# Optimization experiments

Measured on AMD Instinct MI355X. Metric: run time of the kernel, lower is better.

The kernel has to match this reference:

```python
import jax, jax.numpy as jnp
import numpy as np
from jax import lax

B, UD, YD, ZD, H, L, T = 256, 16, 16, 32, 128, 2, 2048


def _lin_params(key, out_dim, in_dim):
    k1, k2 = jax.random.split(key)
    s = 1.0 / np.sqrt(in_dim)
    w = jax.random.uniform(k1, (out_dim, in_dim), minval=-s, maxval=s, dtype=jnp.float32)
    b = jax.random.uniform(k2, (out_dim,), minval=-s, maxval=s, dtype=jnp.float32)
    return w, b


def setup_inputs() -> dict:
    key = jax.random.key(0)
    ks = iter(jax.random.split(key, 24))
    d = {}
    d["u"] = jax.random.normal(next(ks), (B, UD, T), dtype=jnp.float32)
    d["y"] = jax.random.normal(next(ks), (B, YD, T), dtype=jnp.float32)
    d["h0"] = jax.random.uniform(next(ks), (L, B, H), dtype=jnp.float32)  # torch.rand init
    d["phi_u_w1"], d["phi_u_b1"] = _lin_params(next(ks), H, UD)
    d["phi_u_w2"], d["phi_u_b2"] = _lin_params(next(ks), H, H)
    d["dynn_w1"], d["dynn_b1"] = _lin_params(next(ks), H, 2 * H)
    d["dynn_w2"], d["dynn_b2"] = _lin_params(next(ks), H, H)
    d["x_mean_w"], d["x_mean_b"] = _lin_params(next(ks), ZD, H)
    d["phi_x_w1"], d["phi_x_b1"] = _lin_params(next(ks), H, ZD)
    d["phi_x_w2"], d["phi_x_b2"] = _lin_params(next(ks), H, H)
    d["menn_w1"], d["menn_b1"] = _lin_params(next(ks), H, H)
    d["menn_w2"], d["menn_b2"] = _lin_params(next(ks), YD, H)
    s = 1.0 / np.sqrt(H)
    d["gru_wih"] = jax.random.uniform(next(ks), (L, 3 * H, H), minval=-s, maxval=s, dtype=jnp.float32)
    d["gru_whh"] = jax.random.uniform(next(ks), (L, 3 * H, H), minval=-s, maxval=s, dtype=jnp.float32)
    return d


def _mlp(x, w1, b1, w2, b2):
    # Linear -> ReLU -> Linear (torch Linear convention: x @ W.T + b)
    return jax.nn.relu(x @ w1.T + b1) @ w2.T + b2


def _gru_step(h, x_in, wih, whh):
    # h: (L, B, H); x_in: (B, H); nn.GRU with bias=False
    new_h = []
    inp = x_in
    for l in range(L):
        gi = inp @ wih[l].T           # (B, 3H)
        gh = h[l] @ whh[l].T          # (B, 3H)
        i_r, i_z, i_n = jnp.split(gi, 3, axis=-1)
        h_r, h_z, h_n = jnp.split(gh, 3, axis=-1)
        r = jax.nn.sigmoid(i_r + h_r)
        z = jax.nn.sigmoid(i_z + h_z)
        n = jnp.tanh(i_n + r * h_n)
        hl = (1.0 - z) * n + z * h[l]
        new_h.append(hl)
        inp = hl
    return jnp.stack(new_h)


def reference(u, y, h0, phi_u_w1, phi_u_b1, phi_u_w2, phi_u_b2,
              dynn_w1, dynn_b1, dynn_w2, dynn_b2, x_mean_w, x_mean_b,
              phi_x_w1, phi_x_b1, phi_x_w2, phi_x_b2,
              menn_w1, menn_b1, menn_w2, menn_b2, gru_wih, gru_whh):
    # mpnt_wt = -1 branch (0 >= mpnt_wt > -10): pure NN dynamics + measurement
    u_t = jnp.transpose(u, (2, 0, 1))  # (T, B, UD)
    y_t = jnp.transpose(y, (2, 0, 1))  # (T, B, YD)
    # phi_u has no recurrent dependency -> precompute over all timesteps
    pu = _mlp(u_t, phi_u_w1, phi_u_b1, phi_u_w2, phi_u_b2)  # (T, B, H)

    def step(h, inputs):
        pu_t, yt = inputs
        d = _mlp(jnp.concatenate([pu_t, h[-1]], axis=1), dynn_w1, dynn_b1, dynn_w2, dynn_b2)
        x_t = d @ x_mean_w.T + x_mean_b                 # (B, ZD)
        h_new = _gru_step(h, pu_t, gru_wih, gru_whh)
        px = _mlp(x_t, phi_x_w1, phi_x_b1, phi_x_w2, phi_x_b2)
        y_hat = _mlp(px, menn_w1, menn_b1, menn_w2, menn_b2)
        loss_t = jnp.sum((y_hat - yt) ** 2)
        return h_new, loss_t

    _, losses = lax.scan(step, h0, (pu, y_t))
    return jnp.sum(losses)
```

## Files before the change

kernel.cpp:

```cpp
#include <hip/hip_runtime.h>
#include <hip/hip_bf16.h>

#define TT 2048
#define BB 256
#define HH 128
#define UDIM 16
#define YDIM 16
#define ZDIM 32
#define H3 384

typedef __hip_bfloat16 bf16;
typedef _Float16 half2v __attribute__((ext_vector_type(2)));

constexpr int clog2(int x) { return x <= 1 ? 0 : 1 + clog2(x >> 1); }

template <int M_, int K_, int O_, bool RELU_>
__device__ __forceinline__ void rstage(const float* __restrict__ wfrag,
                                       const float* __restrict__ xin, int XS,
                                       float* __restrict__ ps,
                                       const float* __restrict__ bias,
                                       float* __restrict__ outb)
{
    constexpr int F = K_ / O_;
    const int T = threadIdx.x;
    const int jb = T & (M_ / 2 - 1);
    const int o  = T >> clog2(M_ / 2);
#pragma unroll
    for (int r = 0; r < 8; ++r) {
        float a0 = 0.f, a1 = 0.f;
#pragma unroll
        for (int g = 0; g < F; g += 4) {
            const float4 xv = *reinterpret_cast<const float4*>(&xin[r * XS + o * F + g]);
            a0 += xv.x * wfrag[g]     + xv.y * wfrag[g + 1]
                + xv.z * wfrag[g + 2] + xv.w * wfrag[g + 3];
            a1 += xv.x * wfrag[F + g]     + xv.y * wfrag[F + g + 1]
                + xv.z * wfrag[F + g + 2] + xv.w * wfrag[F + g + 3];
        }
        ps[r * 1024 + o * M_ + jb]           = a0;
        ps[r * 1024 + o * M_ + jb + M_ / 2]  = a1;
    }
    __syncthreads();
    for (int oi = T; oi < 8 * M_; oi += 512) {
        const int r = oi >> clog2(M_);
        const int j = oi & (M_ - 1);
        float s = bias[j];
#pragma unroll
        for (int o2 = 0; o2 < O_; ++o2) s += ps[r * 1024 + o2 * M_ + j];
        if (RELU_) s = fmaxf(s, 0.f);
        outb[r * M_ + j] = s;
    }
    __syncthreads();
}

template <int M_, int K_, int O_>
__device__ __forceinline__ void loadw(float* __restrict__ wfrag, const float* __restrict__ Wg)
{
    constexpr int F = K_ / O_;
    const int T = threadIdx.x;
    const int jb = T & (M_ / 2 - 1);
    const int o  = T >> clog2(M_ / 2);
#pragma unroll
    for (int h = 0; h < 2; ++h)
#pragma unroll
        for (int g = 0; g < F; g += 4)
            *reinterpret_cast<float4*>(&wfrag[h * F + g]) =
                *reinterpret_cast<const float4*>(&Wg[(jb + h * (M_ / 2)) * K_ + o * F + g]);
}

template <int M_, int K_, int O_>
__device__ __forceinline__ void loadw_h(half2v* __restrict__ wfrag, const float* __restrict__ Wg)
{
    constexpr int F = K_ / O_;
    const int T = threadIdx.x;
    const int jb = T & (M_ / 2 - 1);
    const int o  = T >> clog2(M_ / 2);
#pragma unroll
    for (int h = 0; h < 2; ++h)
#pragma unroll
        for (int g = 0; g < F / 2; ++g) {
            const float* s = &Wg[(jb + h * (M_ / 2)) * K_ + o * F + 2 * g];
            half2v v; v.x = (_Float16)s[0]; v.y = (_Float16)s[1];
            wfrag[h * (F / 2) + g] = v;
        }
}

template <int M_, int K_, int O_, bool RELU_>
__device__ __forceinline__ void rstage_h(const half2v* __restrict__ wfrag,
                                         const _Float16* __restrict__ xin, int XS,
                                         float* __restrict__ ps,
                                         const float* __restrict__ bias,
                                         _Float16* __restrict__ outb)
{
    constexpr int F = K_ / O_;
    constexpr int FH = F / 2;
    const int T = threadIdx.x;
    const int jb = T & (M_ / 2 - 1);
    const int o  = T >> clog2(M_ / 2);
#pragma unroll
    for (int r = 0; r < 8; ++r) {
        float a0 = 0.f, a1 = 0.f;
        const half2v* xv = reinterpret_cast<const half2v*>(xin + r * XS + o * F);
        if constexpr (FH >= 4) {
#pragma unroll
            for (int g4 = 0; g4 < FH / 4; ++g4) {
                half2v xt[4];
                *reinterpret_cast<float4*>(xt) = reinterpret_cast<const float4*>(xv)[g4];
#pragma unroll
                for (int e = 0; e < 4; ++e) {
                    a0 = __builtin_amdgcn_fdot2(xt[e], wfrag[g4 * 4 + e], a0, false);
                    a1 = __builtin_amdgcn_fdot2(xt[e], wfrag[FH + g4 * 4 + e], a1, false);
                }
            }
        } else {
            half2v xt[2];
            *reinterpret_cast<float2*>(xt) = *reinterpret_cast<const float2*>(xv);
            a0 = __builtin_amdgcn_fdot2(xt[0], wfrag[0], a0, false);
            a0 = __builtin_amdgcn_fdot2(xt[1], wfrag[1], a0, false);
            a1 = __builtin_amdgcn_fdot2(xt[0], wfrag[FH], a1, false);
            a1 = __builtin_amdgcn_fdot2(xt[1], wfrag[FH + 1], a1, false);
        }
        ps[r * 1024 + o * M_ + jb]           = a0;
        ps[r * 1024 + o * M_ + jb + M_ / 2]  = a1;
    }
    __syncthreads();
    for (int oi = T; oi < 8 * M_; oi += 512) {
        const int r = oi >> clog2(M_);
        const int j = oi & (M_ - 1);
        float s = bias[j];
#pragma unroll
        for (int o2 = 0; o2 < O_; ++o2) s += ps[r * 1024 + o2 * M_ + j];
        if (RELU_) s = fmaxf(s, 0.f);
        outb[r * M_ + j] = (_Float16)s;
    }
    __syncthreads();
}

__global__ __launch_bounds__(512, 2) void phi_u_kernel(
    const float* __restrict__ u, const float* __restrict__ w1, const float* __restrict__ b1,
    const float* __restrict__ w2, const float* __restrict__ b2,
    bf16* __restrict__ pu, int s0, int nrows)
{
    __shared__ __align__(16) float ps[8192];
    __shared__ __align__(16) float xc[8 * 16];
    __shared__ __align__(16) float bP[8 * 128];
    __shared__ __align__(16) float bias_l[256];
    const int T = threadIdx.x;
    if (T < 128) { bias_l[T] = b1[T]; bias_l[128 + T] = b2[T]; }
    const int jb = T & 63, o = T >> 6;
    float wa[4];
    wa[0] = w1[jb * 16 + o * 2];        wa[1] = w1[jb * 16 + o * 2 + 1];
    wa[2] = w1[(jb + 64) * 16 + o * 2]; wa[3] = w1[(jb + 64) * 16 + o * 2 + 1];
    float wb[32]; loadw<128, 128, 8>(wb, w2);
    __syncthreads();

    for (int tile = blockIdx.x; tile < nrows / 32; tile += gridDim.x) {
        const int n0 = tile * 32;
        const int b  = s0 + (n0 >> 11);
        const int t0 = n0 & (TT - 1);
#pragma unroll 1
        for (int rb = 0; rb < 4; ++rb) {
            if (T < 128) {
                const int r = T & 7, c = T >> 3;
                xc[r * 16 + c] = u[((size_t)b * UDIM + c) * TT + t0 + rb * 8 + r];
            }
            __syncthreads();
#pragma unroll
            for (int r = 0; r < 8; ++r) {
                const float x0 = xc[r * 16 + o * 2], x1 = xc[r * 16 + o * 2 + 1];
                ps[r * 1024 + o * 128 + jb]      = x0 * wa[0] + x1 * wa[1];
                ps[r * 1024 + o * 128 + jb + 64] = x0 * wa[2] + x1 * wa[3];
            }
            __syncthreads();
            for (int oi = T; oi < 8 * 128; oi += 512) {
                const int r = oi >> 7, j = oi & 127;
                float s = bias_l[j];
#pragma unroll
                for (int o2 = 0; o2 < 8; ++o2) s += ps[r * 1024 + o2 * 128 + j];
                bP[r * 128 + j] = fmaxf(s, 0.f);
            }
            __syncthreads();
            rstage<128, 128, 8, false>(wb, bP, 128, ps, bias_l + 128, bP);
            const int row0 = n0 + rb * 8;
            for (int oi = T; oi < 8 * 128; oi += 512) {
                const int r = oi >> 7, j = oi & 127;
                pu[(size_t)(row0 + r) * HH + j] = __float2bfloat16(bP[r * 128 + j]);
            }
            __syncthreads();
        }
    }
}

__device__ __forceinline__ void gmv(const half2v w[6][16], const _Float16* __restrict__ vb,
                                    int o, float* __restrict__ psL, int psb)
{
    const half2v* vec2 = reinterpret_cast<const half2v*>(vb) + o * 16;
    float a0 = 0.f, a1 = 0.f, a2 = 0.f, a3 = 0.f, a4 = 0.f, a5 = 0.f;
#pragma unroll
    for (int k4 = 0; k4 < 4; ++k4) {
        half2v xt[4];
        *reinterpret_cast<float4*>(xt) = reinterpret_cast<const float4*>(vec2)[k4];
#pragma unroll
        for (int e = 0; e < 4; ++e) {
            const int k = k4 * 4 + e;
            a0 = __builtin_amdgcn_fdot2(xt[e], w[0][k], a0, false);
            a1 = __builtin_amdgcn_fdot2(xt[e], w[1][k], a1, false);
            a2 = __builtin_amdgcn_fdot2(xt[e], w[2][k], a2, false);
            a3 = __builtin_amdgcn_fdot2(xt[e], w[3][k], a3, false);
            a4 = __builtin_amdgcn_fdot2(xt[e], w[4][k], a4, false);
            a5 = __builtin_amdgcn_fdot2(xt[e], w[5][k], a5, false);
        }
    }
    psL[psb]       = a0; psL[psb + 64]  = a1; psL[psb + 128] = a2;
    psL[psb + 192] = a3; psL[psb + 256] = a4; psL[psb + 320] = a5;
}

__global__ __launch_bounds__(512, 2) void gru_fused_kernel(
    const bf16* __restrict__ pu_in,
    const float* __restrict__ wih,
    const float* __restrict__ whh,
    const float* __restrict__ h0_g,
    bf16* __restrict__ hlast,
    int s0)
{
    const int t = threadIdx.x;
    __shared__ __align__(16) _Float16 x0h[HH];
    __shared__ __align__(16) _Float16 x1h[2][HH];
    __shared__ __align__(16) _Float16 h0h[HH];
    __shared__ __align__(16) _Float16 h1h[HH];
    __shared__ __align__(16) float ps[2 * 3072];

    const int g = t >> 6;
    const int m = g >> 2, o = g & 3;
    const int u = t & 63;
    const float* WbaseA = ((m == 0) ? wih : whh);
    const float* WbaseB = WbaseA + (size_t)H3 * HH;
    half2v wA[6][16], wB[6][16];
#pragma unroll
    for (int i = 0; i < 6; ++i) {
        const float* sA = &WbaseA[(u + 64 * i) * HH + o * 32];
        const float* sB = &WbaseB[(u + 64 * i) * HH + o * 32];
#pragma unroll
        for (int k = 0; k < 16; ++k) {
            half2v v; v.x = (_Float16)sA[2 * k]; v.y = (_Float16)sA[2 * k + 1];
            wA[i][k] = v;
            half2v w2; w2.x = (_Float16)sB[2 * k]; w2.y = (_Float16)sB[2 * k + 1];
            wB[i][k] = w2;
        }
    }
    float* psA = ps;
    float* psB = ps + 3072;
    const int psb = o * 768 + m * 384 + u;

    const bf16* xb = pu_in + (size_t)blockIdx.x * TT * HH;
    bf16* ob = hlast + (size_t)blockIdx.x * TT * HH;

    float hreg = 0.f;
    if (t < HH) {
        hreg = h0_g[(size_t)(s0 + blockIdx.x) * HH + t];
        h0h[t] = (_Float16)hreg;
        x0h[t] = (_Float16)__bfloat162float(xb[t]);
    } else if (t < 2 * HH) {
        const int j = t - HH;
        hreg = h0_g[((size_t)BB + s0 + blockIdx.x) * HH + j];
        h1h[j] = (_Float16)hreg;
    }
    __syncthreads();

#pragma unroll 1
    for (int i = 0; i <= TT; ++i) {
        float xnext = 0.f;
        if (t < HH && i + 1 < TT)
            xnext = __bfloat162float(xb[(size_t)(i + 1) * HH + t]);
        if (i < TT)  gmv(wA, (m == 0) ? x0h : h0h, o, psA, psb);
        if (i >= 1)  gmv(wB, (m == 0) ? x1h[(i + 1) & 1] : h1h, o, psB, psb);
        __syncthreads();
        if (t < HH) {
            if (i < TT) {
                const int j = t;
                float gir = 0.f, giz = 0.f, gin = 0.f, ghr = 0.f, ghz = 0.f, ghn = 0.f;
#pragma unroll
                for (int o2 = 0; o2 < 4; ++o2) {
                    const float* pp = psA + o2 * 768;
                    gir += pp[j];        giz += pp[128 + j]; gin += pp[256 + j];
                    ghr += pp[384 + j];  ghz += pp[512 + j]; ghn += pp[640 + j];
                }
                const float rg = 1.f / (1.f + __expf(-(gir + ghr)));
                const float zg = 1.f / (1.f + __expf(-(giz + ghz)));
                const float narg = gin + rg * ghn;
                const float e2 = __expf(2.f * fabsf(narg));
                float ng = 1.f - 2.f / (e2 + 1.f);
                ng = (narg < 0.f) ? -ng : ng;
                const float hn = (1.f - zg) * ng + zg * hreg;
                h0h[j] = (_Float16)hn;
                x1h[i & 1][j] = (_Float16)hn;
                x0h[j] = (_Float16)xnext;
                hreg = hn;
            }
        } else if (t < 2 * HH) {
            if (i >= 1) {
                const int j = t - HH;
                float gir = 0.f, giz = 0.f, gin = 0.f, ghr = 0.f, ghz = 0.f, ghn = 0.f;
#pragma unroll
                for (int o2 = 0; o2 < 4; ++o2) {
                    const float* pp = psB + o2 * 768;
                    gir += pp[j];        giz += pp[128 + j]; gin += pp[256 + j];
                    ghr += pp[384 + j];  ghz += pp[512 + j]; ghn += pp[640 + j];
                }
                const float rg = 1.f / (1.f + __expf(-(gir + ghr)));
                const float zg = 1.f / (1.f + __expf(-(giz + ghz)));
                const float narg = gin + rg * ghn;
                const float e2 = __expf(2.f * fabsf(narg));
                float ng = 1.f - 2.f / (e2 + 1.f);
                ng = (narg < 0.f) ? -ng : ng;
                ob[(size_t)(i - 1) * HH + j] = __float2bfloat16(hreg);
                const float hn = (1.f - zg) * ng + zg * hreg;
                h1h[j] = (_Float16)hn;
                hreg = hn;
            }
        }
        __syncthreads();
    }
}

__device__ __forceinline__ void stage_xc_h(_Float16* __restrict__ xc,
                                           const bf16* __restrict__ pu,
                                           const bf16* __restrict__ hl,
                                           int n0, int rb)
{
    const int T = threadIdx.x;
    const int base = n0 + rb * 8;
#pragma unroll
    for (int i = 0; i < 4; ++i) {
        const int idx = T + i * 512;
        const int r = idx >> 8, k = idx & 255;
        const size_t row = (size_t)(base + r);
        xc[r * 256 + k] = (_Float16)((k < 128) ? __bfloat162float(pu[row * HH + k])
                                               : __bfloat162float(hl[row * HH + (k - 128)]));
    }
}

__global__ __launch_bounds__(512, 2) void head_kernel(
    const bf16* __restrict__ pu, const bf16* __restrict__ hlast, const float* __restrict__ y_g,
    const float* __restrict__ dw1, const float* __restrict__ db1,
    const float* __restrict__ dw2, const float* __restrict__ db2,
    const float* __restrict__ xw, const float* __restrict__ xb,
    const float* __restrict__ pxw1, const float* __restrict__ pxb1,
    const float* __restrict__ pxw2, const float* __restrict__ pxb2,
    const float* __restrict__ mw1, const float* __restrict__ mb1,
    const float* __restrict__ mw2, const float* __restrict__ mb2,
    float* __restrict__ out, int s0, int nrows)
{
    __shared__ __align__(16) float ps[8192];
    __shared__ __align__(16) _Float16 xc[8 * 256];
    __shared__ __align__(16) _Float16 bP[8 * 128];
    __shared__ __align__(16) _Float16 bQ[8 * 128];
    __shared__ __align__(16) _Float16 bX[8 * 32];
    __shared__ __align__(16) float bias_l[688];
    __shared__ float red[8];
    const int T = threadIdx.x;

    if (T < 128) bias_l[T]       = db1[T];
    if (T < 128) bias_l[128 + T] = db2[T];
    if (T < 32)  bias_l[256 + T] = xb[T];
    if (T < 128) bias_l[288 + T] = pxb1[T];
    if (T < 128) bias_l[416 + T] = pxb2[T];
    if (T < 128) bias_l[544 + T] = mb1[T];
    if (T < 16)  bias_l[672 + T] = mb2[T];

    half2v w1[32]; loadw_h<128, 256, 8 >(w1, dw1);
    half2v w2[16]; loadw_h<128, 128, 8 >(w2, dw2);
    half2v w3[4];  loadw_h<32,  128, 32>(w3, xw);
    half2v w4[4];  loadw_h<128, 32,  8 >(w4, pxw1);
    half2v w5[16]; loadw_h<128, 128, 8 >(w5, pxw2);
    half2v w6[16]; loadw_h<128, 128, 8 >(w6, mw1);
    const int jb7 = T & 7, o7 = T >> 3;
    half2v w7a, w7b;
    w7a.x = (_Float16)mw2[jb7 * 128 + 2 * o7];
    w7a.y = (_Float16)mw2[jb7 * 128 + 2 * o7 + 1];
    w7b.x = (_Float16)mw2[(jb7 + 8) * 128 + 2 * o7];
    w7b.y = (_Float16)mw2[(jb7 + 8) * 128 + 2 * o7 + 1];

    float lossreg = 0.f;

    for (int tile = blockIdx.x; tile < nrows / 32; tile += gridDim.x) {
        const int n0 = tile * 32;
        const int b  = s0 + (n0 >> 11);
        const int t0 = n0 & (TT - 1);
        stage_xc_h(xc, pu, hlast, n0, 0);
#pragma unroll 1
        for (int rb = 0; rb < 4; ++rb) {
            __syncthreads();
            rstage_h<128, 256, 8,  true >(w1, xc, 256, ps, bias_l + 0,   bP);
            rstage_h<128, 128, 8,  false>(w2, bP, 128, ps, bias_l + 128, bQ);
            rstage_h<32,  128, 32, false>(w3, bQ, 128, ps, bias_l + 256, bX);
            rstage_h<128, 32,  8,  true >(w4, bX, 32,  ps, bias_l + 288, bP);
            rstage_h<128, 128, 8,  false>(w5, bP, 128, ps, bias_l + 416, bQ);
            rstage_h<128, 128, 8,  true >(w6, bQ, 128, ps, bias_l + 544, bP);
#pragma unroll
            for (int r = 0; r < 8; ++r) {
                const half2v xv = *reinterpret_cast<const half2v*>(&bP[r * 128 + 2 * o7]);
                ps[r * 1024 + o7 * 16 + jb7]     = __builtin_amdgcn_fdot2(xv, w7a, 0.f, false);
                ps[r * 1024 + o7 * 16 + jb7 + 8] = __builtin_amdgcn_fdot2(xv, w7b, 0.f, false);
            }
            if (rb < 3) stage_xc_h(xc, pu, hlast, n0, rb + 1);
            __syncthreads();
            if (T < 128) {
                const int r = T >> 4, j = T & 15;
                float s = bias_l[672 + j];
#pragma unroll
                for (int o2 = 0; o2 < 64; ++o2) s += ps[r * 1024 + o2 * 16 + j];
                const int trow = t0 + rb * 8 + r;
                const float yv = y_g[((size_t)b * YDIM + j) * TT + trow];
                const float d = s - yv;
                lossreg += d * d;
            }
        }
    }
    __syncthreads();
#pragma unroll
    for (int off = 32; off > 0; off >>= 1) lossreg += __shfl_down(lossreg, off, 64);
    if ((T & 63) == 0) red[T >> 6] = lossreg;
    __syncthreads();
    if (T == 0) {
        float s = 0.f;
#pragma unroll
        for (int i = 0; i < 8; ++i) s += red[i];
        atomicAdd(out, s);
    }
}

__global__ void zero_out_kernel(float* o) { o[0] = 0.f; }

extern "C" void kernel_launch(void* const* d_in, const int* in_sizes, int n_in,
                              void* d_out, int out_size, void* d_ws, size_t ws_size,
                              hipStream_t stream)
{
    (void)in_sizes; (void)n_in; (void)out_size;
    const float* u    = (const float*)d_in[0];
    const float* y    = (const float*)d_in[1];
    const float* h0   = (const float*)d_in[2];
    const float* puw1 = (const float*)d_in[3];
    const float* pub1 = (const float*)d_in[4];
    const float* puw2 = (const float*)d_in[5];
    const float* pub2 = (const float*)d_in[6];
    const float* dw1  = (const float*)d_in[7];
    const float* db1  = (const float*)d_in[8];
    const float* dw2  = (const float*)d_in[9];
    const float* db2  = (const float*)d_in[10];
    const float* xw   = (const float*)d_in[11];
    const float* xbi  = (const float*)d_in[12];
    const float* pxw1 = (const float*)d_in[13];
    const float* pxb1 = (const float*)d_in[14];
    const float* pxw2 = (const float*)d_in[15];
    const float* pxb2 = (const float*)d_in[16];
    const float* mw1  = (const float*)d_in[17];
    const float* mb1  = (const float*)d_in[18];
    const float* mw2  = (const float*)d_in[19];
    const float* mb2  = (const float*)d_in[20];
    const float* gwih = (const float*)d_in[21];
    const float* gwhh = (const float*)d_in[22];

    const size_t per_sample = (size_t)TT * HH * 2 * 2;
    int C = BB;
    while (C > 1 && (size_t)C * per_sample > ws_size) C >>= 1;
    bf16* puB = (bf16*)d_ws;
    bf16* hlB = puB + (size_t)C * TT * HH;

    zero_out_kernel<<<1, 1, 0, stream>>>((float*)d_out);
    for (int s0 = 0; s0 < BB; s0 += C) {
        phi_u_kernel<<<512, 512, 0, stream>>>(u, puw1, pub1, puw2, pub2, puB, s0, C * TT);
        gru_fused_kernel<<<C, 512, 0, stream>>>(puB, gwih, gwhh, h0, hlB, s0);
        head_kernel<<<512, 512, 0, stream>>>(puB, hlB, y,
                                             dw1, db1, dw2, db2, xw, xbi,
                                             pxw1, pxb1, pxw2, pxb2,
                                             mw1, mb1, mw2, mb2,
                                             (float*)d_out, s0, C * TT);
    }
}
```

Before: 4.888 ms.

## Replace shared-memory partial-sum reductions with wavefront shuffle reductions

```diff
diff --git a/kernel.cpp b/kernel.cpp
--- a/kernel.cpp
+++ b/kernel.cpp
@@ -68,69 +68,87 @@
 }
 
 template <int M_, int K_, int O_>
-__device__ __forceinline__ void loadw_h(half2v* __restrict__ wfrag, const float* __restrict__ Wg)
+__device__ __forceinline__ void loadw_s(half2v* __restrict__ wfrag, const float* __restrict__ Wg)
 {
     constexpr int F = K_ / O_;
-    const int T = threadIdx.x;
-    const int jb = T & (M_ / 2 - 1);
-    const int o  = T >> clog2(M_ / 2);
-#pragma unroll
-    for (int h = 0; h < 2; ++h)
-#pragma unroll
-        for (int g = 0; g < F / 2; ++g) {
-            const float* s = &Wg[(jb + h * (M_ / 2)) * K_ + o * F + 2 * g];
-            half2v v; v.x = (_Float16)s[0]; v.y = (_Float16)s[1];
-            wfrag[h * (F / 2) + g] = v;
-        }
+    constexpr int FH = F / 2;
+    constexpr int LO = clog2(O_);
+    const int T = threadIdx.x;
+    const int o  = T & (O_ - 1);
+    const int jb = T >> LO;
+#pragma unroll
+    for (int h = 0; h < 2; ++h) {
+        const float* src = Wg + (size_t)(jb + h * (M_ / 2)) * K_;
+        if constexpr (F >= 8) {
+            constexpr int NS = F / 8;
+#pragma unroll
+            for (int s = 0; s < NS; ++s)
+#pragma unroll
+                for (int e = 0; e < 4; ++e) {
+                    const float* p = src + o * 8 + s * (8 * O_) + 2 * e;
+                    half2v v; v.x = (_Float16)p[0]; v.y = (_Float16)p[1];
+                    wfrag[h * FH + s * 4 + e] = v;
+                }
+        } else {
+#pragma unroll
+            for (int e = 0; e < 2; ++e) {
+                const float* p = src + o * 4 + 2 * e;
+                half2v v; v.x = (_Float16)p[0]; v.y = (_Float16)p[1];
+                wfrag[h * FH + e] = v;
+            }
+        }
+    }
 }
 
 template <int M_, int K_, int O_, bool RELU_>
-__device__ __forceinline__ void rstage_h(const half2v* __restrict__ wfrag,
+__device__ __forceinline__ void rstage_s(const half2v* __restrict__ wfrag,
                                          const _Float16* __restrict__ xin, int XS,
-                                         float* __restrict__ ps,
                                          const float* __restrict__ bias,
                                          _Float16* __restrict__ outb)
 {
     constexpr int F = K_ / O_;
     constexpr int FH = F / 2;
-    const int T = threadIdx.x;
-    const int jb = T & (M_ / 2 - 1);
-    const int o  = T >> clog2(M_ / 2);
+    constexpr int LO = clog2(O_);
+    const int T = threadIdx.x;
+    const int o  = T & (O_ - 1);
+    const int jb = T >> LO;
 #pragma unroll
     for (int r = 0; r < 8; ++r) {
         float a0 = 0.f, a1 = 0.f;
-        const half2v* xv = reinterpret_cast<const half2v*>(xin + r * XS + o * F);
-        if constexpr (FH >= 4) {
-#pragma unroll
-            for (int g4 = 0; g4 < FH / 4; ++g4) {
+        if constexpr (F >= 8) {
+            constexpr int NS = F / 8;
+#pragma unroll
+            for (int s = 0; s < NS; ++s) {
                 half2v xt[4];
-                *reinterpret_cast<float4*>(xt) = reinterpret_cast<const float4*>(xv)[g4];
+                *reinterpret_cast<float4*>(xt) =
+                    *reinterpret_cast<const float4*>(xin + r * XS + o * 8 + s * (8 * O_));
 #pragma unroll
                 for (int e = 0; e < 4; ++e) {
-                    a0 = __builtin_amdgcn_fdot2(xt[e], wfrag[g4 * 4 + e], a0, false);
-                    a1 = __builtin_amdgcn_fdot2(xt[e], wfrag[FH + g4 * 4 + e], a1, false);
+                    a0 = __builtin_amdgcn_fdot2(xt[e], wfrag[s * 4 + e], a0, false);
+                    a1 = __builtin_amdgcn_fdot2(xt[e], wfrag[FH + s * 4 + e], a1, false);
                 }
             }
         } else {
             half2v xt[2];
-            *reinterpret_cast<float2*>(xt) = *reinterpret_cast<const float2*>(xv);
+            *reinterpret_cast<float2*>(xt) =
+                *reinterpret_cast<const float2*>(xin + r * XS + o * 4);
             a0 = __builtin_amdgcn_fdot2(xt[0], wfrag[0], a0, false);
             a0 = __builtin_amdgcn_fdot2(xt[1], wfrag[1], a0, false);
             a1 = __builtin_amdgcn_fdot2(xt[0], wfrag[FH], a1, false);
             a1 = __builtin_amdgcn_fdot2(xt[1], wfrag[FH + 1], a1, false);
         }
-        ps[r * 1024 + o * M_ + jb]           = a0;
-        ps[r * 1024 + o * M_ + jb + M_ / 2]  = a1;
-    }
-    __syncthreads();
-    for (int oi = T; oi < 8 * M_; oi += 512) {
-        const int r = oi >> clog2(M_);
-        const int j = oi & (M_ - 1);
-        float s = bias[j];
-#pragma unroll
-        for (int o2 = 0; o2 < O_; ++o2) s += ps[r * 1024 + o2 * M_ + j];
-        if (RELU_) s = fmaxf(s, 0.f);
-        outb[r * M_ + j] = (_Float16)s;
+#pragma unroll
+        for (int s = 1; s < O_; s <<= 1) {
+            a0 += __shfl_xor(a0, s, 64);
+            a1 += __shfl_xor(a1, s, 64);
+        }
+        if (o == 0) {
+            float s0 = a0 + bias[jb];
+            float s1 = a1 + bias[jb + M_ / 2];
+            if (RELU_) { s0 = fmaxf(s0, 0.f); s1 = fmaxf(s1, 0.f); }
+            outb[r * M_ + jb]          = (_Float16)s0;
+            outb[r * M_ + jb + M_ / 2] = (_Float16)s1;
+        }
     }
     __syncthreads();
 }
@@ -190,11 +208,11 @@
     }
 }
 
-__device__ __forceinline__ void gmv(const half2v w[6][16], const _Float16* __restrict__ vb,
-                                    int o, float* __restrict__ psL, int psb)
+__device__ __forceinline__ void gmv_s(const half2v w[6][16], const _Float16* __restrict__ vb,
+                                      int o, float* __restrict__ a)
 {
     const half2v* vec2 = reinterpret_cast<const half2v*>(vb) + o * 16;
-    float a0 = 0.f, a1 = 0.f, a2 = 0.f, a3 = 0.f, a4 = 0.f, a5 = 0.f;
+    a[0] = 0.f; a[1] = 0.f; a[2] = 0.f; a[3] = 0.f; a[4] = 0.f; a[5] = 0.f;
 #pragma unroll
     for (int k4 = 0; k4 < 4; ++k4) {
         half2v xt[4];
@@ -202,16 +220,19 @@
 #pragma unroll
         for (int e = 0; e < 4; ++e) {
             const int k = k4 * 4 + e;
-            a0 = __builtin_amdgcn_fdot2(xt[e], w[0][k], a0, false);
-            a1 = __builtin_amdgcn_fdot2(xt[e], w[1][k], a1, false);
-            a2 = __builtin_amdgcn_fdot2(xt[e], w[2][k], a2, false);
-            a3 = __builtin_amdgcn_fdot2(xt[e], w[3][k], a3, false);
-            a4 = __builtin_amdgcn_fdot2(xt[e], w[4][k], a4, false);
-            a5 = __builtin_amdgcn_fdot2(xt[e], w[5][k], a5, false);
-        }
-    }
-    psL[psb]       = a0; psL[psb + 64]  = a1; psL[psb + 128] = a2;
-    psL[psb + 192] = a3; psL[psb + 256] = a4; psL[psb + 320] = a5;
+            a[0] = __builtin_amdgcn_fdot2(xt[e], w[0][k], a[0], false);
+            a[1] = __builtin_amdgcn_fdot2(xt[e], w[1][k], a[1], false);
+            a[2] = __builtin_amdgcn_fdot2(xt[e], w[2][k], a[2], false);
+            a[3] = __builtin_amdgcn_fdot2(xt[e], w[3][k], a[3], false);
+            a[4] = __builtin_amdgcn_fdot2(xt[e], w[4][k], a[4], false);
+            a[5] = __builtin_amdgcn_fdot2(xt[e], w[5][k], a[5], false);
+        }
+    }
+#pragma unroll
+    for (int j = 0; j < 6; ++j) {
+        a[j] += __shfl_xor(a[j], 1, 64);
+        a[j] += __shfl_xor(a[j], 2, 64);
+    }
 }
 
 __global__ __launch_bounds__(512, 2) void gru_fused_kernel(
@@ -227,29 +248,30 @@
     __shared__ __align__(16) _Float16 x1h[2][HH];
     __shared__ __align__(16) _Float16 h0h[HH];
     __shared__ __align__(16) _Float16 h1h[HH];
-    __shared__ __align__(16) float ps[2 * 3072];
-
+    __shared__ __align__(16) float ps[2 * 768];
+
+    const int lane = t & 63;
+    const int o = lane & 3;
+    const int r16 = lane >> 2;
     const int g = t >> 6;
-    const int m = g >> 2, o = g & 3;
-    const int u = t & 63;
+    const int m = g >> 2, q = g & 3;
+    const int rbase = r16 + 16 * q;
     const float* WbaseA = ((m == 0) ? wih : whh);
     const float* WbaseB = WbaseA + (size_t)H3 * HH;
     half2v wA[6][16], wB[6][16];
 #pragma unroll
-    for (int i = 0; i < 6; ++i) {
-        const float* sA = &WbaseA[(u + 64 * i) * HH + o * 32];
-        const float* sB = &WbaseB[(u + 64 * i) * HH + o * 32];
+    for (int i6 = 0; i6 < 6; ++i6) {
+        const float* sA = WbaseA + (size_t)(rbase + 64 * i6) * HH + o * 32;
+        const float* sB = WbaseB + (size_t)(rbase + 64 * i6) * HH + o * 32;
 #pragma unroll
         for (int k = 0; k < 16; ++k) {
             half2v v; v.x = (_Float16)sA[2 * k]; v.y = (_Float16)sA[2 * k + 1];
-            wA[i][k] = v;
-            half2v w2; w2.x = (_Float16)sB[2 * k]; w2.y = (_Float16)sB[2 * k + 1];
-            wB[i][k] = w2;
-        }
-    }
-    float* psA = ps;
-    float* psB = ps + 3072;
-    const int psb = o * 768 + m * 384 + u;
+            wA[i6][k] = v;
+            half2v u2; u2.x = (_Float16)sB[2 * k]; u2.y = (_Float16)sB[2 * k + 1];
+            wB[i6][k] = u2;
+        }
+    }
+    const int psb = m * 384 + rbase;
 
     const bf16* xb = pu_in + (size_t)blockIdx.x * TT * HH;
     bf16* ob = hlast + (size_t)blockIdx.x * TT * HH;
@@ -271,19 +293,26 @@
         float xnext = 0.f;
         if (t < HH && i + 1 < TT)
             xnext = __bfloat162float(xb[(size_t)(i + 1) * HH + t]);
-        if (i < TT)  gmv(wA, (m == 0) ? x0h : h0h, o, psA, psb);
-        if (i >= 1)  gmv(wB, (m == 0) ? x1h[(i + 1) & 1] : h1h, o, psB, psb);
+        float a[6], bv[6];
+        if (i < TT)  gmv_s(wA, (m == 0) ? x0h : h0h, o, a);
+        if (i >= 1)  gmv_s(wB, (m == 0) ? x1h[(i + 1) & 1] : h1h, o, bv);
+        if (o < 2) {
+            const int base = psb + o * 192;
+            const float v0 = o ? a[3] : a[0];
+            const float v1 = o ? a[4] : a[1];
+            const float v2 = o ? a[5] : a[2];
+            const float u0 = o ? bv[3] : bv[0];
+            const float u1 = o ? bv[4] : bv[1];
+            const float u2 = o ? bv[5] : bv[2];
+            if (i < TT) { ps[base] = v0; ps[base + 64] = v1; ps[base + 128] = v2; }
+            if (i >= 1) { ps[768 + base] = u0; ps[768 + base + 64] = u1; ps[768 + base + 128] = u2; }
+        }
         __syncthreads();
         if (t < HH) {
             if (i < TT) {
                 const int j = t;
-                float gir = 0.f, giz = 0.f, gin = 0.f, ghr = 0.f, ghz = 0.f, ghn = 0.f;
-#pragma unroll
-                for (int o2 = 0; o2 < 4; ++o2) {
-                    const float* pp = psA + o2 * 768;
-                    gir += pp[j];        giz += pp[128 + j]; gin += pp[256 + j];
-                    ghr += pp[384 + j];  ghz += pp[512 + j]; ghn += pp[640 + j];
-                }
+                const float gir = ps[j],       giz = ps[128 + j], gin = ps[256 + j];
+                const float ghr = ps[384 + j], ghz = ps[512 + j], ghn = ps[640 + j];
                 const float rg = 1.f / (1.f + __expf(-(gir + ghr)));
                 const float zg = 1.f / (1.f + __expf(-(giz + ghz)));
                 const float narg = gin + rg * ghn;
@@ -299,13 +328,8 @@
         } else if (t < 2 * HH) {
             if (i >= 1) {
                 const int j = t - HH;
-                float gir = 0.f, giz = 0.f, gin = 0.f, ghr = 0.f, ghz = 0.f, ghn = 0.f;
-#pragma unroll
-                for (int o2 = 0; o2 < 4; ++o2) {
-                    const float* pp = psB + o2 * 768;
-                    gir += pp[j];        giz += pp[128 + j]; gin += pp[256 + j];
-                    ghr += pp[384 + j];  ghz += pp[512 + j]; ghn += pp[640 + j];
-                }
+                const float gir = ps[768 + j],       giz = ps[896 + j], gin = ps[1024 + j];
+                const float ghr = ps[1152 + j], ghz = ps[1280 + j], ghn = ps[1408 + j];
                 const float rg = 1.f / (1.f + __expf(-(gir + ghr)));
                 const float zg = 1.f / (1.f + __expf(-(giz + ghz)));
                 const float narg = gin + rg * ghn;
@@ -350,7 +374,6 @@
     const float* __restrict__ mw2, const float* __restrict__ mb2,
     float* __restrict__ out, int s0, int nrows)
 {
-    __shared__ __align__(16) float ps[8192];
     __shared__ __align__(16) _Float16 xc[8 * 256];
     __shared__ __align__(16) _Float16 bP[8 * 128];
     __shared__ __align__(16) _Float16 bQ[8 * 128];
@@ -367,18 +390,18 @@
     if (T < 128) bias_l[544 + T] = mb1[T];
     if (T < 16)  bias_l[672 + T] = mb2[T];
 
-    half2v w1[32]; loadw_h<128, 256, 8 >(w1, dw1);
-    half2v w2[16]; loadw_h<128, 128, 8 >(w2, dw2);
-    half2v w3[4];  loadw_h<32,  128, 32>(w3, xw);
-    half2v w4[4];  loadw_h<128, 32,  8 >(w4, pxw1);
-    half2v w5[16]; loadw_h<128, 128, 8 >(w5, pxw2);
-    half2v w6[16]; loadw_h<128, 128, 8 >(w6, mw1);
-    const int jb7 = T & 7, o7 = T >> 3;
+    half2v w1[32]; loadw_s<128, 256, 8 >(w1, dw1);
+    half2v w2[16]; loadw_s<128, 128, 8 >(w2, dw2);
+    half2v w3[4];  loadw_s<32,  128, 32>(w3, xw);
+    half2v w4[4];  loadw_s<128, 32,  8 >(w4, pxw1);
+    half2v w5[16]; loadw_s<128, 128, 8 >(w5, pxw2);
+    half2v w6[16]; loadw_s<128, 128, 8 >(w6, mw1);
+    const int o7 = T & 63, j7 = T >> 6;
     half2v w7a, w7b;
-    w7a.x = (_Float16)mw2[jb7 * 128 + 2 * o7];
-    w7a.y = (_Float16)mw2[jb7 * 128 + 2 * o7 + 1];
-    w7b.x = (_Float16)mw2[(jb7 + 8) * 128 + 2 * o7];
-    w7b.y = (_Float16)mw2[(jb7 + 8) * 128 + 2 * o7 + 1];
+    w7a.x = (_Float16)mw2[j7 * 128 + 2 * o7];
+    w7a.y = (_Float16)mw2[j7 * 128 + 2 * o7 + 1];
+    w7b.x = (_Float16)mw2[(j7 + 8) * 128 + 2 * o7];
+    w7b.y = (_Float16)mw2[(j7 + 8) * 128 + 2 * o7 + 1];
 
     float lossreg = 0.f;
 
@@ -387,36 +410,38 @@
         const int b  = s0 + (n0 >> 11);
         const int t0 = n0 & (TT - 1);
         stage_xc_h(xc, pu, hlast, n0, 0);
+        __syncthreads();
 #pragma unroll 1
         for (int rb = 0; rb < 4; ++rb) {
-            __syncthreads();
-            rstage_h<128, 256, 8,  true >(w1, xc, 256, ps, bias_l + 0,   bP);
-            rstage_h<128, 128, 8,  false>(w2, bP, 128, ps, bias_l + 128, bQ);
-            rstage_h<32,  128, 32, false>(w3, bQ, 128, ps, bias_l + 256, bX);
-            rstage_h<128, 32,  8,  true >(w4, bX, 32,  ps, bias_l + 288, bP);
-            rstage_h<128, 128, 8,  false>(w5, bP, 128, ps, bias_l + 416, bQ);
-            rstage_h<128, 128, 8,  true >(w6, bQ, 128, ps, bias_l + 544, bP);
+            rstage_s<128, 256, 8,  true >(w1, xc, 256, bias_l + 0,   bP);
+            if (rb < 3) stage_xc_h(xc, pu, hlast, n0, rb + 1);
+            rstage_s<128, 128, 8,  false>(w2, bP, 128, bias_l + 128, bQ);
+            rstage_s<32,  128, 32, false>(w3, bQ, 128, bias_l + 256, bX);
+            rstage_s<128, 32,  8,  true >(w4, bX, 32,  bias_l + 288, bP);
+            rstage_s<128, 128, 8,  false>(w5, bP, 128, bias_l + 416, bQ);
+            rstage_s<128, 128, 8,  true >(w6, bQ, 128, bias_l + 544, bP);
 #pragma unroll
             for (int r = 0; r < 8; ++r) {
                 const half2v xv = *reinterpret_cast<const half2v*>(&bP[r * 128 + 2 * o7]);
-                ps[r * 1024 + o7 * 16 + jb7]     = __builtin_amdgcn_fdot2(xv, w7a, 0.f, false);
-                ps[r * 1024 + o7 * 16 + jb7 + 8] = __builtin_amdgcn_fdot2(xv, w7b, 0.f, false);
-            }
-            if (rb < 3) stage_xc_h(xc, pu, hlast, n0, rb + 1);
+                float a0 = __builtin_amdgcn_fdot2(xv, w7a, 0.f, false);
+                float a1 = __builtin_amdgcn_fdot2(xv, w7b, 0.f, false);
+#pragma unroll
+                for (int s = 1; s < 64; s <<= 1) {
+                    a0 += __shfl_xor(a0, s, 64);
+                    a1 += __shfl_xor(a1, s, 64);
+                }
+                if (o7 == 0) {
+                    const int trow = t0 + rb * 8 + r;
+                    const float y0 = y_g[((size_t)b * YDIM + j7) * TT + trow];
+                    const float y1 = y_g[((size_t)b * YDIM + j7 + 8) * TT + trow];
+                    const float d0 = a0 + bias_l[672 + j7] - y0;
+                    const float d1 = a1 + bias_l[680 + j7] - y1;
+                    lossreg += d0 * d0 + d1 * d1;
+                }
+            }
             __syncthreads();
-            if (T < 128) {
-                const int r = T >> 4, j = T & 15;
-                float s = bias_l[672 + j];
-#pragma unroll
-                for (int o2 = 0; o2 < 64; ++o2) s += ps[r * 1024 + o2 * 16 + j];
-                const int trow = t0 + rb * 8 + r;
-                const float yv = y_g[((size_t)b * YDIM + j) * TT + trow];
-                const float d = s - yv;
-                lossreg += d * d;
-            }
-        }
-    }
-    __syncthreads();
+        }
+    }
 #pragma unroll
     for (int off = 32; off > 0; off >>= 1) lossreg += __shfl_down(lossreg, off, 64);
     if ((T & 63) == 0) red[T >> 6] = lossreg;
```

Measured after the change: 7.873 ms. +61.0%, slower.

## Collapse three consecutive linear layers in head into one precomputed matrix

Applied to the files above, without the earlier changes.

```diff
diff --git a/kernel.cpp b/kernel.cpp
--- a/kernel.cpp
+++ b/kernel.cpp
@@ -133,6 +133,41 @@
         outb[r * M_ + j] = (_Float16)s;
     }
     __syncthreads();
+}
+
+__global__ __launch_bounds__(512) void pre1_kernel(
+    const float* __restrict__ pxw1, const float* __restrict__ xw, float* __restrict__ A)
+{
+    const int T = threadIdx.x;
+    for (int idx = T; idx < 128 * 128; idx += 512) {
+        const int j = idx >> 7, m = idx & 127;
+        float s = 0.f;
+#pragma unroll
+        for (int z = 0; z < 32; ++z) s += pxw1[j * 32 + z] * xw[z * 128 + m];
+        A[idx] = s;
+    }
+}
+
+__global__ __launch_bounds__(512) void pre2_kernel(
+    const float* __restrict__ A, const float* __restrict__ dw2,
+    const float* __restrict__ db2, const float* __restrict__ pxw1,
+    const float* __restrict__ xb, const float* __restrict__ pxb1,
+    float* __restrict__ wC, float* __restrict__ bC)
+{
+    const int idx = blockIdx.x * 512 + threadIdx.x;
+    if (blockIdx.x < 32) {
+        const int j = idx >> 7, k = idx & 127;
+        float s = 0.f;
+        for (int m = 0; m < 128; ++m) s += A[j * 128 + m] * dw2[m * 128 + k];
+        wC[idx] = s;
+    } else if (threadIdx.x < 128) {
+        const int j = threadIdx.x;
+        float s = pxb1[j];
+        for (int m = 0; m < 128; ++m) s += A[j * 128 + m] * db2[m];
+#pragma unroll
+        for (int z = 0; z < 32; ++z) s += pxw1[j * 32 + z] * xb[z];
+        bC[j] = s;
+    }
 }
 
 __global__ __launch_bounds__(512, 2) void phi_u_kernel(
@@ -342,9 +377,7 @@
 __global__ __launch_bounds__(512, 2) void head_kernel(
     const bf16* __restrict__ pu, const bf16* __restrict__ hlast, const float* __restrict__ y_g,
     const float* __restrict__ dw1, const float* __restrict__ db1,
-    const float* __restrict__ dw2, const float* __restrict__ db2,
-    const float* __restrict__ xw, const float* __restrict__ xb,
-    const float* __restrict__ pxw1, const float* __restrict__ pxb1,
+    const float* __restrict__ wC, const float* __restrict__ bC,
     const float* __restrict__ pxw2, const float* __restrict__ pxb2,
     const float* __restrict__ mw1, const float* __restrict__ mb1,
     const float* __restrict__ mw2, const float* __restrict__ mb2,
@@ -354,23 +387,18 @@
     __shared__ __align__(16) _Float16 xc[8 * 256];
     __shared__ __align__(16) _Float16 bP[8 * 128];
     __shared__ __align__(16) _Float16 bQ[8 * 128];
-    __shared__ __align__(16) _Float16 bX[8 * 32];
-    __shared__ __align__(16) float bias_l[688];
+    __shared__ __align__(16) float bias_l[528];
     __shared__ float red[8];
     const int T = threadIdx.x;
 
     if (T < 128) bias_l[T]       = db1[T];
-    if (T < 128) bias_l[128 + T] = db2[T];
-    if (T < 32)  bias_l[256 + T] = xb[T];
-    if (T < 128) bias_l[288 + T] = pxb1[T];
-    if (T < 128) bias_l[416 + T] = pxb2[T];
-    if (T < 128) bias_l[544 + T] = mb1[T];
-    if (T < 16)  bias_l[672 + T] = mb2[T];
+    if (T < 128) bias_l[128 + T] = bC[T];
+    if (T < 128) bias_l[256 + T] = pxb2[T];
+    if (T < 128) bias_l[384 + T] = mb1[T];
+    if (T < 16)  bias_l[512 + T] = mb2[T];
 
     half2v w1[32]; loadw_h<128, 256, 8 >(w1, dw1);
-    half2v w2[16]; loadw_h<128, 128, 8 >(w2, dw2);
-    half2v w3[4];  loadw_h<32,  128, 32>(w3, xw);
-    half2v w4[4];  loadw_h<128, 32,  8 >(w4, pxw1);
+    half2v wc[16]; loadw_h<128, 128, 8 >(wc, wC);
     half2v w5[16]; loadw_h<128, 128, 8 >(w5, pxw2);
     half2v w6[16]; loadw_h<128, 128, 8 >(w6, mw1);
     const int jb7 = T & 7, o7 = T >> 3;
@@ -390,15 +418,13 @@
 #pragma unroll 1
         for (int rb = 0; rb < 4; ++rb) {
             __syncthreads();
-            rstage_h<128, 256, 8,  true >(w1, xc, 256, ps, bias_l + 0,   bP);
-            rstage_h<128, 128, 8,  false>(w2, bP, 128, ps, bias_l + 128, bQ);
-            rstage_h<32,  128, 32, false>(w3, bQ, 128, ps, bias_l + 256, bX);
-            rstage_h<128, 32,  8,  true >(w4, bX, 32,  ps, bias_l + 288, bP);
-            rstage_h<128, 128, 8,  false>(w5, bP, 128, ps, bias_l + 416, bQ);
-            rstage_h<128, 128, 8,  true >(w6, bQ, 128, ps, bias_l + 544, bP);
+            rstage_h<128, 256, 8, true >(w1, xc, 256, ps, bias_l + 0,   bP);
+            rstage_h<128, 128, 8, true >(wc, bP, 128, ps, bias_l + 128, bQ);
+            rstage_h<128, 128, 8, false>(w5, bQ, 128, ps, bias_l + 256, bP);
+            rstage_h<128, 128, 8, true >(w6, bP, 128, ps, bias_l + 384, bQ);
 #pragma unroll
             for (int r = 0; r < 8; ++r) {
-                const half2v xv = *reinterpret_cast<const half2v*>(&bP[r * 128 + 2 * o7]);
+                const half2v xv = *reinterpret_cast<const half2v*>(&bQ[r * 128 + 2 * o7]);
                 ps[r * 1024 + o7 * 16 + jb7]     = __builtin_amdgcn_fdot2(xv, w7a, 0.f, false);
                 ps[r * 1024 + o7 * 16 + jb7 + 8] = __builtin_amdgcn_fdot2(xv, w7b, 0.f, false);
             }
@@ -406,7 +432,7 @@
             __syncthreads();
             if (T < 128) {
                 const int r = T >> 4, j = T & 15;
-                float s = bias_l[672 + j];
+                float s = bias_l[512 + j];
 #pragma unroll
                 for (int o2 = 0; o2 < 64; ++o2) s += ps[r * 1024 + o2 * 16 + j];
                 const int trow = t0 + rb * 8 + r;
@@ -460,20 +486,25 @@
     const float* gwih = (const float*)d_in[21];
     const float* gwhh = (const float*)d_in[22];
 
+    const size_t extra = (3 * 16384 + 128) * sizeof(float);
     const size_t per_sample = (size_t)TT * HH * 2 * 2;
     int C = BB;
-    while (C > 1 && (size_t)C * per_sample > ws_size) C >>= 1;
+    while (C > 1 && (size_t)C * per_sample + extra > ws_size) C >>= 1;
     bf16* puB = (bf16*)d_ws;
     bf16* hlB = puB + (size_t)C * TT * HH;
+    float* Aw = (float*)((char*)d_ws + (size_t)C * per_sample);
+    float* wC = Aw + 16384;
+    float* bC = wC + 16384;
 
     zero_out_kernel<<<1, 1, 0, stream>>>((float*)d_out);
+    pre1_kernel<<<1, 512, 0, stream>>>(pxw1, xw, Aw);
+    pre2_kernel<<<33, 512, 0, stream>>>(Aw, dw2, db2, pxw1, xbi, pxb1, wC, bC);
     for (int s0 = 0; s0 < BB; s0 += C) {
         phi_u_kernel<<<512, 512, 0, stream>>>(u, puw1, pub1, puw2, pub2, puB, s0, C * TT);
         gru_fused_kernel<<<C, 512, 0, stream>>>(puB, gwih, gwhh, h0, hlB, s0);
         head_kernel<<<512, 512, 0, stream>>>(puB, hlB, y,
-                                             dw1, db1, dw2, db2, xw, xbi,
-                                             pxw1, pxb1, pxw2, pxb2,
-                                             mw1, mb1, mw2, mb2,
+                                             dw1, db1, wC, bC,
+                                             pxw2, pxb2, mw1, mb1, mw2, mb2,
                                              (float*)d_out, s0, C * TT);
     }
 }
```

Measured after the change: 7.180 ms. 46.9% more time.

## Fold three consecutive linear layers into one precomputed weight matrix

Applied to the files above, without the earlier changes.

```diff
diff --git a/kernel.cpp b/kernel.cpp
--- a/kernel.cpp
+++ b/kernel.cpp
@@ -354,23 +354,56 @@
     __shared__ __align__(16) _Float16 xc[8 * 256];
     __shared__ __align__(16) _Float16 bP[8 * 128];
     __shared__ __align__(16) _Float16 bQ[8 * 128];
-    __shared__ __align__(16) _Float16 bX[8 * 32];
-    __shared__ __align__(16) float bias_l[688];
+    __shared__ __align__(16) float bias_l[528];
     __shared__ float red[8];
     const int T = threadIdx.x;
 
     if (T < 128) bias_l[T]       = db1[T];
-    if (T < 128) bias_l[128 + T] = db2[T];
-    if (T < 32)  bias_l[256 + T] = xb[T];
-    if (T < 128) bias_l[288 + T] = pxb1[T];
-    if (T < 128) bias_l[416 + T] = pxb2[T];
-    if (T < 128) bias_l[544 + T] = mb1[T];
-    if (T < 16)  bias_l[672 + T] = mb2[T];
+    if (T < 128) bias_l[256 + T] = pxb2[T];
+    if (T < 128) bias_l[384 + T] = mb1[T];
+    if (T < 16)  bias_l[512 + T] = mb2[T];
+
+    for (int idx = T; idx < 4096; idx += 512) {
+        const int z = idx >> 7, k = idx & 127;
+        float s = 0.f;
+        for (int m2 = 0; m2 < 128; ++m2) s += xw[z * 128 + m2] * dw2[m2 * 128 + k];
+        ps[idx] = s;
+    }
+    if (T < 32) {
+        float c = xb[T];
+        for (int m2 = 0; m2 < 128; ++m2) c += xw[T * 128 + m2] * db2[m2];
+        ps[4096 + T] = c;
+    }
+    __syncthreads();
+    half2v wc[16];
+    {
+        const int jbw = T & 63, ow = T >> 6;
+#pragma unroll
+        for (int h = 0; h < 2; ++h) {
+            const int j = jbw + h * 64;
+#pragma unroll
+            for (int gg = 0; gg < 8; ++gg) {
+                const int k0 = ow * 16 + 2 * gg;
+                float s0 = 0.f, s1 = 0.f;
+#pragma unroll
+                for (int z = 0; z < 32; ++z) {
+                    const float p = pxw1[j * 32 + z];
+                    s0 += p * ps[z * 128 + k0];
+                    s1 += p * ps[z * 128 + k0 + 1];
+                }
+                half2v v; v.x = (_Float16)s0; v.y = (_Float16)s1;
+                wc[h * 8 + gg] = v;
+            }
+        }
+    }
+    if (T < 128) {
+        float s = pxb1[T];
+#pragma unroll
+        for (int z = 0; z < 32; ++z) s += pxw1[T * 32 + z] * ps[4096 + z];
+        bias_l[128 + T] = s;
+    }
 
     half2v w1[32]; loadw_h<128, 256, 8 >(w1, dw1);
-    half2v w2[16]; loadw_h<128, 128, 8 >(w2, dw2);
-    half2v w3[4];  loadw_h<32,  128, 32>(w3, xw);
-    half2v w4[4];  loadw_h<128, 32,  8 >(w4, pxw1);
     half2v w5[16]; loadw_h<128, 128, 8 >(w5, pxw2);
     half2v w6[16]; loadw_h<128, 128, 8 >(w6, mw1);
     const int jb7 = T & 7, o7 = T >> 3;
@@ -390,15 +423,13 @@
 #pragma unroll 1
         for (int rb = 0; rb < 4; ++rb) {
             __syncthreads();
-            rstage_h<128, 256, 8,  true >(w1, xc, 256, ps, bias_l + 0,   bP);
-            rstage_h<128, 128, 8,  false>(w2, bP, 128, ps, bias_l + 128, bQ);
-            rstage_h<32,  128, 32, false>(w3, bQ, 128, ps, bias_l + 256, bX);
-            rstage_h<128, 32,  8,  true >(w4, bX, 32,  ps, bias_l + 288, bP);
-            rstage_h<128, 128, 8,  false>(w5, bP, 128, ps, bias_l + 416, bQ);
-            rstage_h<128, 128, 8,  true >(w6, bQ, 128, ps, bias_l + 544, bP);
+            rstage_h<128, 256, 8, true >(w1, xc, 256, ps, bias_l + 0,   bP);
+            rstage_h<128, 128, 8, true >(wc, bP, 128, ps, bias_l + 128, bQ);
+            rstage_h<128, 128, 8, false>(w5, bQ, 128, ps, bias_l + 256, bP);
+            rstage_h<128, 128, 8, true >(w6, bP, 128, ps, bias_l + 384, bQ);
 #pragma unroll
             for (int r = 0; r < 8; ++r) {
-                const half2v xv = *reinterpret_cast<const half2v*>(&bP[r * 128 + 2 * o7]);
+                const half2v xv = *reinterpret_cast<const half2v*>(&bQ[r * 128 + 2 * o7]);
                 ps[r * 1024 + o7 * 16 + jb7]     = __builtin_amdgcn_fdot2(xv, w7a, 0.f, false);
                 ps[r * 1024 + o7 * 16 + jb7 + 8] = __builtin_amdgcn_fdot2(xv, w7b, 0.f, false);
             }
@@ -406,7 +437,7 @@
             __syncthreads();
             if (T < 128) {
                 const int r = T >> 4, j = T & 15;
-                float s = bias_l[672 + j];
+                float s = bias_l[512 + j];
 #pragma unroll
                 for (int o2 = 0; o2 < 64; ++o2) s += ps[r * 1024 + o2 * 16 + j];
                 const int trow = t0 + rb * 8 + r;
```

After: 4.828 ms. About the same (-1.2%).
